# Kernel tuning notes

Measured on AMD Instinct MI355X. Metric: run time of the kernel, lower is better.

The kernel has to match this reference:

```python
import jax, jax.numpy as jnp
import numpy as np


def setup_inputs() -> dict:
    key = jax.random.key(0)
    k1, k2, k3 = jax.random.split(key, 3)
    B, C, H, Wd, p = 64, 3, 448, 448, 28
    x = jax.random.normal(k1, (B, C, H, Wd), dtype=jnp.float32)
    W = jax.random.normal(k2, (3, 3, p, p), dtype=jnp.float32) * 0.02
    b = jax.random.normal(k3, (3,), dtype=jnp.float32) * 0.02
    return {"x": x, "W": W, "b": b, "patch_size": p}


def reference(x, W, b, patch_size):
    # Conv2d(3->3, kernel=stride=patch_size) == blockwise contraction over each patch.
    B, C, H, Wd = x.shape
    p = patch_size
    Hp, Wp = H // p, Wd // p
    N = Hp * Wp
    # [B, C, Hp, p, Wp, p]
    xr = x.reshape(B, C, Hp, p, Wp, p)
    # patches: [B, 3(out), Hp, Wp]
    patches = jnp.einsum('bchiwj,ocij->bohw', xr, W) + b[None, :, None, None]
    # Bilinear upsample of a 1x1 map is a constant broadcast; mean over channels
    # commutes with the broadcast, so compute channel-mean first then broadcast.
    m = patches.mean(axis=1)  # [B, Hp, Wp]
    out = jnp.broadcast_to(m.reshape(B, N, 1, 1), (B, N, p, p))
    return out
```

## Files before the change

kernel.cpp:

```cpp
#include <hip/hip_runtime.h>


#define BLOCK 448

__global__ __launch_bounds__(BLOCK) void patchify_kernel(
    const float* __restrict__ x, const float* __restrict__ W,
    const float* __restrict__ bias, float* __restrict__ out) {
  const int blk = blockIdx.x;
  const int b   = blk >> 4;
  const int hp  = blk & 15;

  __shared__ float  sWm[2352];
  __shared__ float4 scol[4][112];
  __shared__ float  sm[16];
  __shared__ float  sBm;

  const int t = threadIdx.x;

  for (int i = t; i < 2352; i += BLOCK)
    sWm[i] = (W[i] + W[2352 + i] + W[4704 + i]) * (1.0f / 3.0f);
  if (t == 0) sBm = (bias[0] + bias[1] + bias[2]) * (1.0f / 3.0f);
  __syncthreads();

  const int q  = t % 112;
  const int r0 = t / 112;
  const int jm = (4 * q) % 28;

  float4 acc = make_float4(0.f, 0.f, 0.f, 0.f);
  #pragma unroll
  for (int r = r0; r < 84; r += 4) {
    const int c = r / 28;
    const int i = r % 28;
    const float4* row = reinterpret_cast<const float4*>(
        x + ((size_t)(b * 3 + c) * 448 + (size_t)(hp * 28 + i)) * 448);
    const float4 v = row[q];
    const float* w = &sWm[c * 784 + i * 28 + jm];
    acc.x += v.x * w[0];
    acc.y += v.y * w[1];
    acc.z += v.z * w[2];
    acc.w += v.w * w[3];
  }
  scol[r0][q] = acc;
  __syncthreads();

  if (t < 16) {
    float s = 0.f;
    for (int g = 0; g < 4; ++g) {
      #pragma unroll
      for (int k = 0; k < 7; ++k) {
        const float4 v = scol[g][t * 7 + k];
        s += (v.x + v.y) + (v.z + v.w);
      }
    }
    sm[t] = s + sBm;
  }
  __syncthreads();

  float4* o4 = reinterpret_cast<float4*>(out + (size_t)(b * 256 + hp * 16) * 784);
  for (int idx = t; idx < 3136; idx += BLOCK) {
    const float m = sm[idx / 196];
    o4[idx] = make_float4(m, m, m, m);
  }
}

extern "C" void kernel_launch(void* const* d_in, const int* in_sizes, int n_in,
                              void* d_out, int out_size, void* d_ws, size_t ws_size,
                              hipStream_t stream) {
  const float* x    = (const float*)d_in[0];
  const float* W    = (const float*)d_in[1];
  const float* bias = (const float*)d_in[2];
  float* out = (float*)d_out;
  patchify_kernel<<<dim3(1024), dim3(BLOCK), 0, stream>>>(x, W, bias, out);
}
```

Baseline: 250.2 us.

## Assign one wavefront per patch with precomputed gather offsets and nontemporal stores

Restructures the work split so each 64-lane wavefront computes one patch. Lanes gather float4s through a shared-memory table of byte offsets, reduce with xor shuffles, and write the broadcast output with nontemporal stores. This removes the two block-level reduction barriers and the serial 16-thread reduction of the old row-strip layout. In exchange every block repeats the channel-averaged weight table setup, now over 4096 blocks instead of 1024, and the input reads become 112-byte patch rows instead of full contiguous image rows.

Result: faster. 236.2 us (-5.6%).

```diff
diff --git a/kernel.cpp b/kernel.cpp
--- a/kernel.cpp
+++ b/kernel.cpp
@@ -1,65 +1,72 @@
 #include <hip/hip_runtime.h>
 
 
-#define BLOCK 448
+#define BLOCK 256
+#define NF 588
+
+typedef float f32x4 __attribute__((ext_vector_type(4)));
 
 __global__ __launch_bounds__(BLOCK) void patchify_kernel(
     const float* __restrict__ x, const float* __restrict__ W,
     const float* __restrict__ bias, float* __restrict__ out) {
-  const int blk = blockIdx.x;
-  const int b   = blk >> 4;
-  const int hp  = blk & 15;
-
-  __shared__ float  sWm[2352];
-  __shared__ float4 scol[4][112];
-  __shared__ float  sm[16];
-  __shared__ float  sBm;
+  __shared__ float4 sW4[NF];
+  __shared__ int    sT[NF];
 
   const int t = threadIdx.x;
 
-  for (int i = t; i < 2352; i += BLOCK)
-    sWm[i] = (W[i] + W[2352 + i] + W[4704 + i]) * (1.0f / 3.0f);
-  if (t == 0) sBm = (bias[0] + bias[1] + bias[2]) * (1.0f / 3.0f);
-  __syncthreads();
-
-  const int q  = t % 112;
-  const int r0 = t / 112;
-  const int jm = (4 * q) % 28;
-
-  float4 acc = make_float4(0.f, 0.f, 0.f, 0.f);
-  #pragma unroll
-  for (int r = r0; r < 84; r += 4) {
-    const int c = r / 28;
-    const int i = r % 28;
-    const float4* row = reinterpret_cast<const float4*>(
-        x + ((size_t)(b * 3 + c) * 448 + (size_t)(hp * 28 + i)) * 448);
-    const float4 v = row[q];
-    const float* w = &sWm[c * 784 + i * 28 + jm];
-    acc.x += v.x * w[0];
-    acc.y += v.y * w[1];
-    acc.z += v.z * w[2];
-    acc.w += v.w * w[3];
-  }
-  scol[r0][q] = acc;
-  __syncthreads();
-
-  if (t < 16) {
-    float s = 0.f;
-    for (int g = 0; g < 4; ++g) {
-      #pragma unroll
-      for (int k = 0; k < 7; ++k) {
-        const float4 v = scol[g][t * 7 + k];
-        s += (v.x + v.y) + (v.z + v.w);
-      }
-    }
-    sm[t] = s + sBm;
+  for (int f = t; f < NF; f += BLOCK) {
+    const float4 a = reinterpret_cast<const float4*>(W)[f];
+    const float4 g = reinterpret_cast<const float4*>(W)[f + NF];
+    const float4 h = reinterpret_cast<const float4*>(W)[f + 2 * NF];
+    sW4[f] = make_float4((a.x + g.x + h.x) * (1.f / 3.f),
+                         (a.y + g.y + h.y) * (1.f / 3.f),
+                         (a.z + g.z + h.z) * (1.f / 3.f),
+                         (a.w + g.w + h.w) * (1.f / 3.f));
+    const int c   = f / 196;
+    const int rem = f - c * 196;
+    const int i   = rem / 7;
+    const int j4  = rem - i * 7;
+    sT[f] = (c * 200704 + i * 448 + j4 * 4) * 4;
   }
   __syncthreads();
 
-  float4* o4 = reinterpret_cast<float4*>(out + (size_t)(b * 256 + hp * 16) * 784);
-  for (int idx = t; idx < 3136; idx += BLOCK) {
-    const float m = sm[idx / 196];
-    o4[idx] = make_float4(m, m, m, m);
+  const int lane = t & 63;
+  const int P    = blockIdx.x * 4 + (t >> 6);
+  const int b    = P >> 8;
+  const int rem  = P & 255;
+  const int hp   = rem >> 4;
+  const int wp   = rem & 15;
+
+  const char* xbase = reinterpret_cast<const char*>(
+      x + (size_t)b * 602112 + (size_t)(hp * 28) * 448 + wp * 28);
+
+  float s = 0.f;
+  #pragma unroll
+  for (int it = 0; it < 9; ++it) {
+    const int f = it * 64 + lane;
+    const float4 v = *reinterpret_cast<const float4*>(xbase + sT[f]);
+    const float4 w = sW4[f];
+    s += v.x * w.x + v.y * w.y + v.z * w.z + v.w * w.w;
+  }
+  {
+    const int f = 576 + lane;
+    if (f < NF) {
+      const float4 v = *reinterpret_cast<const float4*>(xbase + sT[f]);
+      const float4 w = sW4[f];
+      s += v.x * w.x + v.y * w.y + v.z * w.z + v.w * w.w;
+    }
+  }
+
+  #pragma unroll
+  for (int m = 32; m >= 1; m >>= 1) s += __shfl_xor(s, m, 64);
+  s += (bias[0] + bias[1] + bias[2]) * (1.f / 3.f);
+
+  f32x4* o4 = reinterpret_cast<f32x4*>(out + (size_t)P * 784);
+  const f32x4 val = {s, s, s, s};
+  #pragma unroll
+  for (int it = 0; it < 4; ++it) {
+    const int idx = it * 64 + lane;
+    if (idx < 196) __builtin_nontemporal_store(val, o4 + idx);
   }
 }
 
@@ -70,5 +77,5 @@
   const float* W    = (const float*)d_in[1];
   const float* bias = (const float*)d_in[2];
   float* out = (float*)d_out;
-  patchify_kernel<<<dim3(1024), dim3(BLOCK), 0, stream>>>(x, W, bias, out);
+  patchify_kernel<<<dim3(4096), dim3(BLOCK), 0, stream>>>(x, W, bias, out);
 }
```
